# Optimization experiments

Measured on AMD Instinct MI355X. Metric: run time of the kernel, lower is better.

The kernel has to match this reference:

```python
import jax, jax.numpy as jnp
import numpy as np

E, H, B, S = 1024, 16, 8, 512
D = E // H
GRU_BIAS = 2.0  # config['gru_bias']
LN_EPS = 1e-5


def _pos_encoding(seq_len, dim):
    # Transformer-XL style relative positions seq_len-1 .. 0
    pos = jnp.arange(seq_len - 1, -1, -1, dtype=jnp.float32)
    inv_freq = 1.0 / (10000.0 ** (jnp.arange(0, dim, 2, dtype=jnp.float32) / dim))
    ang = pos[:, None] * inv_freq[None, :]              # [S, E/2]
    return jnp.concatenate([jnp.sin(ang), jnp.cos(ang)], axis=-1)  # [S, E]


def _layer_norm(x, g, b):
    m = x.mean(-1, keepdims=True)
    v = ((x - m) ** 2).mean(-1, keepdims=True)
    return (x - m) * jax.lax.rsqrt(v + LN_EPS) * g + b


def _rel_shift(x):
    # x: [B, H, S, S] -> Transformer-XL relative shift
    b, h, s, _ = x.shape
    x = jnp.pad(x, ((0, 0), (0, 0), (0, 0), (1, 0)))
    x = x.reshape(b, h, s + 1, s)[:, :, 1:, :]
    return x


def _gru_gate(x, y, Wr, Ur, Wz, Uz, Wg, Ug):
    # GTrXL gating: r, z gates + candidate h; z biased toward identity by GRU_BIAS
    r = jax.nn.sigmoid(y @ Wr.T + x @ Ur.T)
    z = jax.nn.sigmoid(y @ Wz.T + x @ Uz.T - GRU_BIAS)
    h = jnp.tanh(y @ Wg.T + (r * x) @ Ug.T)
    return (1.0 - z) * x + z * h


def setup_inputs() -> dict:
    rng = jax.random.key(0)
    ks = iter(jax.random.split(rng, 64))
    W = lambda *shape: jax.random.normal(next(ks), shape, jnp.float32) * 0.02
    inp = {
        "query": jax.random.normal(next(ks), (B, S, E), jnp.float32),
        "key": jax.random.normal(next(ks), (B, S, E), jnp.float32),
        "value": jax.random.normal(next(ks), (B, S, E), jnp.float32),
        "mask": jnp.tril(jnp.ones((S, S), dtype=bool)),
        "ln1_g": jnp.ones((E,), jnp.float32), "ln1_b": jnp.zeros((E,), jnp.float32),
        "ln2_g": jnp.ones((E,), jnp.float32), "ln2_b": jnp.zeros((E,), jnp.float32),
        "Wq": W(E, E), "bq": jnp.zeros((E,), jnp.float32),
        "Wk": W(E, E), "bk": jnp.zeros((E,), jnp.float32),
        "Wv": W(E, E), "bv": jnp.zeros((E,), jnp.float32),
        "Wp": W(E, E),
        "Wo": W(E, E), "bo": jnp.zeros((E,), jnp.float32),
        "u_bias": W(H, D), "v_bias": W(H, D),
        "g1_Wr": W(E, E), "g1_Ur": W(E, E), "g1_Wz": W(E, E),
        "g1_Uz": W(E, E), "g1_Wg": W(E, E), "g1_Ug": W(E, E),
        "g2_Wr": W(E, E), "g2_Ur": W(E, E), "g2_Wz": W(E, E),
        "g2_Uz": W(E, E), "g2_Wg": W(E, E), "g2_Ug": W(E, E),
        "fc_W": W(E, E), "fc_b": jnp.zeros((E,), jnp.float32),
    }
    return inp


def reference(query, key, value, mask,
              ln1_g, ln1_b, ln2_g, ln2_b,
              Wq, bq, Wk, bk, Wv, bv, Wp, Wo, bo, u_bias, v_bias,
              g1_Wr, g1_Ur, g1_Wz, g1_Uz, g1_Wg, g1_Ug,
              g2_Wr, g2_Ur, g2_Wz, g2_Uz, g2_Wg, g2_Ug,
              fc_W, fc_b):
    b, s, e = query.shape
    norm_q = _layer_norm(query, ln1_g, ln1_b)
    norm_k = _layer_norm(key, ln1_g, ln1_b)

    q = (norm_q @ Wq.T + bq).reshape(b, s, H, D)
    k = (norm_k @ Wk.T + bk).reshape(b, s, H, D)
    v = (norm_k @ Wv.T + bv).reshape(b, s, H, D)
    r = (_pos_encoding(s, e) @ Wp.T).reshape(s, H, D)      # relative pos keys

    # content term (q + u) k^T and position term (q + v) R^T with rel-shift
    AC = jnp.einsum('bshd,bthd->bhst', q + u_bias, k)
    BD = _rel_shift(jnp.einsum('bshd,thd->bhst', q + v_bias, r))
    score = (AC + BD) / jnp.sqrt(jnp.float32(D))
    score = jnp.where(mask[None, None, :, :], score, jnp.float32(-1e9))
    attn = jax.nn.softmax(score, axis=-1)
    Y = jnp.einsum('bhst,bthd->bshd', attn, v).reshape(b, s, e) @ Wo.T + bo

    out = _gru_gate(query, Y, g1_Wr, g1_Ur, g1_Wz, g1_Uz, g1_Wg, g1_Ug)
    Ef = jax.nn.relu(_layer_norm(out, ln2_g, ln2_b) @ fc_W.T + fc_b)
    out = _gru_gate(out, Ef, g2_Wr, g2_Ur, g2_Wz, g2_Uz, g2_Wg, g2_Ug)
    return out
```

## Files before the change

kernel.cpp:

```cpp
#include <hip/hip_runtime.h>

typedef unsigned short u16;
typedef __attribute__((ext_vector_type(8))) short short8;
typedef __attribute__((ext_vector_type(4))) float f32x4;

#define DEVFN __device__ __forceinline__

constexpr int Bc = 8, Sc = 512, Ec = 1024, Hc = 16, Dc = 64;

DEVFN u16 f2b(float f) {
  union { float f; unsigned u; } a; a.f = f;
  unsigned u = a.u;
  u += 0x7fffu + ((u >> 16) & 1u);
  return (u16)(u >> 16);
}
DEVFN float b2f(u16 h) {
  union { unsigned u; float f; } a; a.u = ((unsigned)h) << 16; return a.f;
}
DEVFN unsigned pack2(float a, float b) {
  return (unsigned)f2b(a) | ((unsigned)f2b(b) << 16);
}
DEVFN float wred_sum(float v) {
  #pragma unroll
  for (int o = 32; o; o >>= 1) v += __shfl_xor(v, o, 64);
  return v;
}
DEVFN void gload16(const void* g, void* l) {
  __builtin_amdgcn_global_load_lds(
      (const __attribute__((address_space(1))) void*)g,
      (__attribute__((address_space(3))) void*)l, 16, 0, 0);
}

struct PtrBundle { const float* src[18]; u16* dst[18]; };

__global__ __launch_bounds__(256) void cvtw_kernel(PtrBundle pb)
{
  int w = blockIdx.y;
  int i = blockIdx.x * 256 + threadIdx.x;
  float4 v = ((const float4*)pb.src[w])[i];
  uint2 o; o.x = pack2(v.x, v.y); o.y = pack2(v.z, v.w);
  ((uint2*)pb.dst[w])[i] = o;
}

struct GemmSeg {
  const u16* A1; const u16* A2;
  const u16* W1; const u16* W2;
  const float* bias;
  const float* bu; const float* bv;
  const u16* xB;
  const float* xF;
  const u16* zB;
  u16* o16a; u16* o16b;
  float* oF;
  int epi;
};
struct GemmDesc { GemmSeg seg[3]; };

template<int TN>
__global__ __launch_bounds__(256) void gemm_f(GemmDesc dd)
{
  constexpr int NI = TN / 32;
  constexpr int BPS = 1024 / TN;
  __shared__ u16 lA[4][128 * 32];
  __shared__ u16 lB[4][TN * 32];
  const int tid = threadIdx.x;

  const GemmSeg s = dd.seg[blockIdx.y / BPS];
  const int n0 = (blockIdx.y % BPS) * TN;
  const int m0 = blockIdx.x * 128;
  const int wid = tid >> 6, lane = tid & 63;
  const int wm = (wid >> 1) * 64, wn = (wid & 1) * (TN / 2);
  const int c15 = lane & 15, g = lane >> 4;
  const int arow = tid >> 2;
  const int ac8 = (((tid & 3) ^ ((tid >> 3) & 3))) * 8;
  const int gs8 = (g ^ ((c15 >> 1) & 3)) * 8;

  f32x4 acc[4][NI];
  #pragma unroll
  for (int mi = 0; mi < 4; ++mi)
    #pragma unroll
    for (int ni = 0; ni < NI; ++ni) acc[mi][ni] = {0.f, 0.f, 0.f, 0.f};

  const int nst = (s.A2 ? 2 : 1) * 32;

  auto stage = [&](int buf, int st) {
    int sg = st >> 5, k0 = (st & 31) << 5;
    const u16* Abase = (sg ? s.A2 : s.A1) + (size_t)m0 * 1024;
    const u16* Wbase = (sg ? s.W2 : s.W1) + (size_t)n0 * 1024;
    gload16(Abase + (size_t)arow * 1024 + k0 + ac8,        &lA[buf][tid * 8]);
    gload16(Abase + (size_t)(arow + 64) * 1024 + k0 + ac8, &lA[buf][2048 + tid * 8]);
    gload16(Wbase + (size_t)arow * 1024 + k0 + ac8,        &lB[buf][tid * 8]);
    if constexpr (TN == 128)
      gload16(Wbase + (size_t)(arow + 64) * 1024 + k0 + ac8, &lB[buf][2048 + tid * 8]);
  };

  stage(0, 0);
  stage(1, 1);
  stage(2, 2);

  for (int st = 0; st < nst; ++st) {
    const int cur = st & 3;
    if (st + 2 < nst) {
      if constexpr (TN == 128) asm volatile("s_waitcnt vmcnt(8)" ::: "memory");
      else                     asm volatile("s_waitcnt vmcnt(6)" ::: "memory");
    } else if (st + 1 < nst) {
      if constexpr (TN == 128) asm volatile("s_waitcnt vmcnt(4)" ::: "memory");
      else                     asm volatile("s_waitcnt vmcnt(3)" ::: "memory");
    } else {
      asm volatile("s_waitcnt vmcnt(0)" ::: "memory");
    }
    __builtin_amdgcn_s_barrier();
    __builtin_amdgcn_sched_barrier(0);

    short8 afr[4], bfr[NI];
    #pragma unroll
    for (int mi = 0; mi < 4; ++mi)
      afr[mi] = *(const short8*)&lA[cur][(wm + mi * 16 + c15) * 32 + gs8];
    #pragma unroll
    for (int ni = 0; ni < NI; ++ni)
      bfr[ni] = *(const short8*)&lB[cur][(wn + ni * 16 + c15) * 32 + gs8];

    if (st + 3 < nst) stage((st + 3) & 3, st + 3);

    #pragma unroll
    for (int mi = 0; mi < 4; ++mi)
      #pragma unroll
      for (int ni = 0; ni < NI; ++ni)
        acc[mi][ni] = __builtin_amdgcn_mfma_f32_16x16x32_bf16(
            afr[mi], bfr[ni], acc[mi][ni], 0, 0, 0);
  }

  const int colb = n0 + wn + c15;
  const int rowb = m0 + wm + (lane >> 4) * 4;
  #pragma unroll
  for (int ni = 0; ni < NI; ++ni) {
    int col = colb + ni * 16;
    float bb = s.bias ? s.bias[col] : 0.f;
    float bu = 0.f, bvv = 0.f;
    if (s.epi == 1) { bu = s.bu[col]; bvv = s.bv[col]; }
    int hI = col >> 6, dI = col & 63;
    int kcd = (dI >> 5) & 1, gd = (dI >> 3) & 3, ed = dI & 7;
    int ntd = dI >> 4, c15d = dI & 15;
    #pragma unroll
    for (int mi = 0; mi < 4; ++mi) {
      int row0 = rowb + mi * 16;
      size_t off0 = (size_t)row0 * 1024 + col;
      float v4[4];
      #pragma unroll
      for (int q = 0; q < 4; ++q) v4[q] = acc[mi][ni][q] + bb;
      switch (s.epi) {
        case 0:
          #pragma unroll
          for (int q = 0; q < 4; ++q) s.o16a[off0 + (size_t)q * 1024] = f2b(v4[q]);
          break;
        case 1:
          #pragma unroll
          for (int q = 0; q < 4; ++q) {
            int ri = row0 + q;
            size_t off = ((size_t)hI << 18) +
                         (((size_t)(((ri >> 4) * 2 + kcd) * 16 + (ri & 15)) * 4 + gd) << 3) + ed;
            s.o16a[off] = f2b((v4[q] + bu)  * 0.125f);
            s.o16b[off] = f2b((v4[q] + bvv) * 0.125f);
          }
          break;
        case 2:
          #pragma unroll
          for (int q = 0; q < 4; ++q) s.o16a[off0 + (size_t)q * 1024] = f2b(v4[q]);
          break;
        case 3:
          #pragma unroll
          for (int q = 0; q < 4; ++q) {
            size_t off = off0 + (size_t)q * 1024;
            float sg1 = 1.f / (1.f + __expf(-v4[q]));
            s.o16a[off] = f2b(sg1 * b2f(s.xB[off]));
          }
          break;
        case 4:
          #pragma unroll
          for (int q = 0; q < 4; ++q) {
            size_t off = off0 + (size_t)q * 1024;
            float z = 1.f / (1.f + __expf(-(b2f(s.zB[off]) - 2.f)));
            float r = (1.f - z) * s.xF[off] + z * tanhf(v4[q]);
            s.oF[off] = r;
            if (s.o16a) s.o16a[off] = f2b(r);
          }
          break;
        case 5:
          #pragma unroll
          for (int q = 0; q < 4; ++q) s.o16a[off0 + (size_t)q * 1024] = f2b(fmaxf(v4[q], 0.f));
          break;
        case 6: {
          int bI = row0 >> 9, j = row0 & 511;
          int kt = j >> 6, jj = j & 63;
          int kcj = jj >> 5, gj = (jj >> 3) & 3, e0 = jj & 7;
          size_t off = ((size_t)((bI * 16 + hI) * 8 + kt) << 12) +
                       (((size_t)((ntd * 2 + kcj) * 16 + c15d) * 4 + gj) << 3) + e0;
          uint2 o; o.x = pack2(v4[0], v4[1]); o.y = pack2(v4[2], v4[3]);
          *(uint2*)(s.o16a + off) = o;
        } break;
        case 7:
          #pragma unroll
          for (int q = 0; q < 4; ++q) {
            int rj = row0 + q;
            int bI = rj >> 9, kt = (rj >> 6) & 7, jr = rj & 63;
            size_t off = ((size_t)((bI * 16 + hI) * 8 + kt) << 12) +
                         (((size_t)(((jr >> 4) * 2 + kcd) * 16 + (jr & 15)) * 4 + gd) << 3) + ed;
            s.o16a[off] = f2b(v4[q]);
          }
          break;
        case 8:
          #pragma unroll
          for (int q = 0; q < 4; ++q) {
            int t = row0 + q;
            size_t off = ((size_t)hI << 14) +
                         (((size_t)(((t >> 4) * 2 + kcd) * 16 + (t & 15)) * 4 + gd) << 3) + ed;
            s.o16a[off] = f2b(v4[q]);
          }
          break;
      }
    }
  }
}

__global__ __launch_bounds__(256) void ln_kernel(
    const float* __restrict__ x, const float* __restrict__ g,
    const float* __restrict__ bb, u16* __restrict__ out,
    u16* __restrict__ out2)
{
  const int row = blockIdx.x, t = threadIdx.x;
  float4 xv = ((const float4*)x)[(size_t)row * 256 + t];
  float s  = xv.x + xv.y + xv.z + xv.w;
  float s2 = xv.x * xv.x + xv.y * xv.y + xv.z * xv.z + xv.w * xv.w;
  s = wred_sum(s); s2 = wred_sum(s2);
  __shared__ float sh[8];
  int wid = t >> 6, lane = t & 63;
  if (lane == 0) { sh[wid] = s; sh[4 + wid] = s2; }
  __syncthreads();
  s  = sh[0] + sh[1] + sh[2] + sh[3];
  s2 = sh[4] + sh[5] + sh[6] + sh[7];
  float mean = s * (1.f / 1024.f);
  float var  = s2 * (1.f / 1024.f) - mean * mean;
  float rstd = rsqrtf(var + 1e-5f);
  float4 gv = ((const float4*)g)[t];
  float4 bv = ((const float4*)bb)[t];
  uint2 o;
  o.x = pack2((xv.x - mean) * rstd * gv.x + bv.x,
              (xv.y - mean) * rstd * gv.y + bv.y);
  o.y = pack2((xv.z - mean) * rstd * gv.z + bv.z,
              (xv.w - mean) * rstd * gv.w + bv.w);
  *(uint2*)&out[(size_t)row * 1024 + t * 4] = o;
  if (out2) {
    uint2 o2; o2.x = pack2(xv.x, xv.y); o2.y = pack2(xv.z, xv.w);
    *(uint2*)&out2[(size_t)row * 1024 + t * 4] = o2;
  }
}

__global__ __launch_bounds__(256) void posenc_kernel(u16* __restrict__ out)
{
  int idx = blockIdx.x * 256 + threadIdx.x;
  int i = idx >> 9, f = idx & 511;
  float pos = (float)(Sc - 1 - i);
  float invf = expf((float)f * -0.017988946039016f);
  float ang = pos * invf;
  out[(size_t)i * 1024 + f]       = f2b(sinf(ang));
  out[(size_t)i * 1024 + 512 + f] = f2b(cosf(ang));
}

__global__ __launch_bounds__(256) void attn_mfma(
    const u16* __restrict__ quF, const u16* __restrict__ qvF,
    const u16* __restrict__ PK, const u16* __restrict__ PVT,
    const u16* __restrict__ RF, u16* __restrict__ out)
{
  __shared__ u16 lK[2][4096];
  __shared__ u16 lVT[2][4096];
  __shared__ u16 PW[4][16 * 72];

  const int tid = threadIdx.x;
  const int wave = tid >> 6, lane = tid & 63;
  const int g = lane >> 4, c15 = lane & 15;
  const int x = blockIdx.x;
  const int h = blockIdx.y, b = blockIdx.z;
  const int qA = x, qB = 7 - x;

  const size_t pkbase = (size_t)(b * 16 + h) << 15;
  const size_t qhead  = (size_t)h << 18;
  const size_t rhead  = (size_t)h << 14;
  const size_t bh_off = ((size_t)b * Sc) * Ec + h * Dc;
  const int fchunk  = (c15 * 4 + g) * 8;
  const int fchunkS = (c15 * 4 + (g ^ ((c15 >> 1) & 3))) * 8;
  const int src8 = (tid ^ ((tid >> 3) & 3)) * 8;

  u16* pw = PW[wave];

  auto stage = [&](int buf, int kt) {
    const u16* ks = PK  + pkbase + ((size_t)kt << 12);
    const u16* vs = PVT + pkbase + ((size_t)kt << 12);
    gload16(ks + src8,        &lK[buf][tid * 8]);
    gload16(ks + 2048 + src8, &lK[buf][2048 + tid * 8]);
    gload16(vs + src8,        &lVT[buf][tid * 8]);
    gload16(vs + 2048 + src8, &lVT[buf][2048 + tid * 8]);
  };

  short8 qa[2], va[2];
  int i0w = qA * 64 + wave * 16;
  {
    int i16g = b * 32 + (i0w >> 4);
    #pragma unroll
    for (int kc = 0; kc < 2; ++kc) {
      size_t off = qhead + ((size_t)(i16g * 2 + kc) * 64) * 8 + fchunk;
      qa[kc] = *(const short8*)(quF + off);
      va[kc] = *(const short8*)(qvF + off);
    }
  }

  f32x4 oacc[4];
  #pragma unroll
  for (int t = 0; t < 4; ++t) oacc[t] = {0.f, 0.f, 0.f, 0.f};
  float m[4], l[4];
  #pragma unroll
  for (int q = 0; q < 4; ++q) { m[q] = -1e30f; l[q] = 0.f; }

  stage(0, 0);
  asm volatile("s_waitcnt vmcnt(0)" ::: "memory");
  __syncthreads();

  for (int s2 = 0; s2 < 9; ++s2) {
    const int buf = s2 & 1;
    const int kt = (s2 <= x) ? s2 : (s2 - x - 1);
    const int j0 = kt * 64;
    if (s2 < 8) {
      int ns = s2 + 1;
      stage(buf ^ 1, (ns <= x) ? ns : (ns - x - 1));
    }

    f32x4 ac[4];
    #pragma unroll
    for (int t = 0; t < 4; ++t) ac[t] = {0.f, 0.f, 0.f, 0.f};
    __builtin_amdgcn_s_setprio(1);
    #pragma unroll
    for (int kc = 0; kc < 2; ++kc)
      #pragma unroll
      for (int nt = 0; nt < 4; ++nt) {
        short8 kb = *(const short8*)&lK[buf][(nt * 2 + kc) * 512 + fchunkS];
        ac[nt] = __builtin_amdgcn_mfma_f32_16x16x32_bf16(qa[kc], kb, ac[nt], 0, 0, 0);
      }

    const int t016 = (496 - i0w + j0) >> 4;
    f32x4 e5[5];
    #pragma unroll
    for (int t = 0; t < 5; ++t) e5[t] = {0.f, 0.f, 0.f, 0.f};
    #pragma unroll
    for (int kc = 0; kc < 2; ++kc)
      #pragma unroll
      for (int nt = 0; nt < 5; ++nt) {
        int t16 = t016 + nt; t16 = t16 > 31 ? 31 : t16;
        short8 rb = *(const short8*)(RF + rhead + (size_t)(t16 * 2 + kc) * 512 + fchunk);
        e5[nt] = __builtin_amdgcn_mfma_f32_16x16x32_bf16(va[kc], rb, e5[nt], 0, 0, 0);
      }
    __builtin_amdgcn_s_setprio(0);

    float rot[5][4];
    #pragma unroll
    for (int q = 0; q < 4; ++q) {
      int src = (lane & 48) | ((15 - (g * 4 + q) + c15) & 15);
      #pragma unroll
      for (int nt = 0; nt < 5; ++nt)
        rot[nt][q] = __shfl(e5[nt][q], src, 64);
    }

    float s[4][4];
    #pragma unroll
    for (int ct = 0; ct < 4; ++ct) {
      int jcol = j0 + ct * 16 + c15;
      #pragma unroll
      for (int q = 0; q < 4; ++q) {
        int r = g * 4 + q;
        int u = 15 - r + c15;
        float bd = (u >> 4) ? rot[ct + 1][q] : rot[ct][q];
        float sv = ac[ct][q] + bd;
        s[ct][q] = (jcol <= i0w + r) ? sv : -1e30f;
      }
    }

    float mnew[4], csc[4];
    #pragma unroll
    for (int q = 0; q < 4; ++q) {
      float mx = fmaxf(fmaxf(s[0][q], s[1][q]), fmaxf(s[2][q], s[3][q]));
      #pragma unroll
      for (int o = 8; o; o >>= 1) mx = fmaxf(mx, __shfl_xor(mx, o, 64));
      mnew[q] = fmaxf(m[q], mx);
      csc[q] = __expf(m[q] - mnew[q]);
      m[q] = mnew[q];
    }
    float rs[4] = {0.f, 0.f, 0.f, 0.f};
    float p[4][4];
    #pragma unroll
    for (int ct = 0; ct < 4; ++ct)
      #pragma unroll
      for (int q = 0; q < 4; ++q) {
        p[ct][q] = __expf(s[ct][q] - mnew[q]);
        rs[q] += p[ct][q];
      }
    #pragma unroll
    for (int q = 0; q < 4; ++q) {
      float t = rs[q];
      #pragma unroll
      for (int o = 8; o; o >>= 1) t += __shfl_xor(t, o, 64);
      l[q] = l[q] * csc[q] + t;
      #pragma unroll
      for (int ct = 0; ct < 4; ++ct) oacc[ct][q] *= csc[q];
    }

    #pragma unroll
    for (int ct = 0; ct < 4; ++ct)
      #pragma unroll
      for (int q = 0; q < 4; ++q)
        pw[(g * 4 + q) * 72 + ct * 16 + c15] = f2b(p[ct][q]);

    __builtin_amdgcn_s_setprio(1);
    #pragma unroll
    for (int kc = 0; kc < 2; ++kc) {
      short8 pa = *(const short8*)&pw[c15 * 72 + kc * 32 + g * 8];
      #pragma unroll
      for (int nt = 0; nt < 4; ++nt) {
        short8 vb8 = *(const short8*)&lVT[buf][(nt * 2 + kc) * 512 + fchunkS];
        oacc[nt] = __builtin_amdgcn_mfma_f32_16x16x32_bf16(pa, vb8, oacc[nt], 0, 0, 0);
      }
    }
    __builtin_amdgcn_s_setprio(0);

    if (s2 == x) {
      #pragma unroll
      for (int q = 0; q < 4; ++q) {
        float rl = 1.f / l[q];
        size_t ro = bh_off + (size_t)(i0w + g * 4 + q) * Ec;
        #pragma unroll
        for (int ct = 0; ct < 4; ++ct)
          out[ro + ct * 16 + c15] = f2b(oacc[ct][q] * rl);
      }
      i0w = qB * 64 + wave * 16;
      int i16g = b * 32 + (i0w >> 4);
      #pragma unroll
      for (int kc = 0; kc < 2; ++kc) {
        size_t off = qhead + ((size_t)(i16g * 2 + kc) * 64) * 8 + fchunk;
        qa[kc] = *(const short8*)(quF + off);
        va[kc] = *(const short8*)(qvF + off);
      }
      #pragma unroll
      for (int t = 0; t < 4; ++t) oacc[t] = {0.f, 0.f, 0.f, 0.f};
      #pragma unroll
      for (int q = 0; q < 4; ++q) { m[q] = -1e30f; l[q] = 0.f; }
    }

    asm volatile("s_waitcnt vmcnt(0)" ::: "memory");
    __syncthreads();
  }

  #pragma unroll
  for (int q = 0; q < 4; ++q) {
    float rl = 1.f / l[q];
    size_t ro = bh_off + (size_t)(i0w + g * 4 + q) * Ec;
    #pragma unroll
    for (int ct = 0; ct < 4; ++ct)
      out[ro + ct * 16 + c15] = f2b(oacc[ct][q] * rl);
  }
}

extern "C" void kernel_launch(void* const* d_in, const int* in_sizes, int n_in,
                              void* d_out, int out_size, void* d_ws, size_t ws_size,
                              hipStream_t stream) {
  (void)in_sizes; (void)n_in; (void)out_size; (void)ws_size;

  const float* query = (const float*)d_in[0];
  const float* key   = (const float*)d_in[1];
  const float* ln1_g = (const float*)d_in[4];
  const float* ln1_b = (const float*)d_in[5];
  const float* ln2_g = (const float*)d_in[6];
  const float* ln2_b = (const float*)d_in[7];
  const float* Wq = (const float*)d_in[8];   const float* bq = (const float*)d_in[9];
  const float* Wk = (const float*)d_in[10];  const float* bk = (const float*)d_in[11];
  const float* Wv = (const float*)d_in[12];  const float* bv_in = (const float*)d_in[13];
  const float* Wp = (const float*)d_in[14];
  const float* Wo = (const float*)d_in[15];  const float* bo = (const float*)d_in[16];
  const float* u_bias = (const float*)d_in[17];
  const float* v_bias = (const float*)d_in[18];
  const float* fc_W = (const float*)d_in[31]; const float* fc_b = (const float*)d_in[32];

  const size_t MB = 1ull << 20;
  char* ws = (char*)d_ws;
  u16* wb[18];
  for (int i = 0; i < 18; ++i) wb[i] = (u16*)(ws + (size_t)i * 2 * MB);
  u16*   normq16 = (u16*)(ws + 36 * MB);
  u16*   normk16 = (u16*)(ws + 44 * MB);
  u16*   xq16    = (u16*)(ws + 52 * MB);
  u16*   pos16   = (u16*)(ws + 60 * MB);
  u16*   rF16    = (u16*)(ws + 61 * MB);
  u16*   quF16   = (u16*)(ws + 62 * MB);
  u16*   qvF16   = (u16*)(ws + 70 * MB);
  u16*   pk16    = (u16*)(ws + 78 * MB);
  u16*   pvt16   = (u16*)(ws + 86 * MB);
  float* out1    = (float*)(ws + 94 * MB);
  u16*   att16   = normq16;
  u16*   Y16     = normk16;
  u16*   rx16    = normq16;
  u16*   out116  = quF16;
  u16*   Ef16    = qvF16;
  u16*   ln2o16  = xq16;
  u16*   tB16    = pk16;

  PtrBundle pb;
  const float* wsrc[18] = {Wq, Wk, Wv, Wp, Wo, fc_W,
                           (const float*)d_in[19], (const float*)d_in[20],
                           (const float*)d_in[21], (const float*)d_in[22],
                           (const float*)d_in[23], (const float*)d_in[24],
                           (const float*)d_in[25], (const float*)d_in[26],
                           (const float*)d_in[27], (const float*)d_in[28],
                           (const float*)d_in[29], (const float*)d_in[30]};
  for (int i = 0; i < 18; ++i) { pb.src[i] = wsrc[i]; pb.dst[i] = wb[i]; }
  cvtw_kernel<<<dim3(1024, 18), 256, 0, stream>>>(pb);

  ln_kernel<<<4096, 256, 0, stream>>>(query, ln1_g, ln1_b, normq16, xq16);
  ln_kernel<<<4096, 256, 0, stream>>>(key,   ln1_g, ln1_b, normk16, nullptr);
  posenc_kernel<<<1024, 256, 0, stream>>>(pos16);

  GemmSeg z{}; GemmDesc d;

  d.seg[0] = z; d.seg[0].A1 = normq16; d.seg[0].W1 = wb[0]; d.seg[0].bias = bq;
  d.seg[0].bu = u_bias; d.seg[0].bv = v_bias;
  d.seg[0].o16a = quF16; d.seg[0].o16b = qvF16; d.seg[0].epi = 1;
  d.seg[1] = z; d.seg[1].A1 = normk16; d.seg[1].W1 = wb[1]; d.seg[1].bias = bk;
  d.seg[1].o16a = pk16; d.seg[1].epi = 7;
  d.seg[2] = z; d.seg[2].A1 = normk16; d.seg[2].W1 = wb[2]; d.seg[2].bias = bv_in;
  d.seg[2].o16a = pvt16; d.seg[2].epi = 6;
  gemm_f<128><<<dim3(32, 24), 256, 0, stream>>>(d);

  d.seg[0] = z; d.seg[0].A1 = pos16; d.seg[0].W1 = wb[3];
  d.seg[0].o16a = rF16; d.seg[0].epi = 8;
  gemm_f<64><<<dim3(4, 16), 256, 0, stream>>>(d);

  attn_mfma<<<dim3(4, 16, 8), 256, 0, stream>>>(quF16, qvF16, pk16, pvt16,
                                                rF16, att16);

  d.seg[0] = z; d.seg[0].A1 = att16; d.seg[0].W1 = wb[4]; d.seg[0].bias = bo;
  d.seg[0].o16a = Y16; d.seg[0].epi = 0;
  gemm_f<64><<<dim3(32, 16), 256, 0, stream>>>(d);

  d.seg[0] = z; d.seg[0].A1 = Y16; d.seg[0].A2 = xq16;
  d.seg[0].W1 = wb[6]; d.seg[0].W2 = wb[7];
  d.seg[0].xB = xq16; d.seg[0].o16a = rx16; d.seg[0].epi = 3;
  d.seg[1] = z; d.seg[1].A1 = Y16; d.seg[1].A2 = xq16;
  d.seg[1].W1 = wb[8]; d.seg[1].W2 = wb[9];
  d.seg[1].o16a = tB16; d.seg[1].epi = 2;
  gemm_f<128><<<dim3(32, 16), 256, 0, stream>>>(d);

  d.seg[0] = z; d.seg[0].A1 = Y16; d.seg[0].A2 = rx16;
  d.seg[0].W1 = wb[10]; d.seg[0].W2 = wb[11];
  d.seg[0].xF = query; d.seg[0].zB = tB16;
  d.seg[0].oF = out1; d.seg[0].o16a = out116; d.seg[0].epi = 4;
  gemm_f<64><<<dim3(32, 16), 256, 0, stream>>>(d);

  ln_kernel<<<4096, 256, 0, stream>>>(out1, ln2_g, ln2_b, ln2o16, nullptr);
  d.seg[0] = z; d.seg[0].A1 = ln2o16; d.seg[0].W1 = wb[5]; d.seg[0].bias = fc_b;
  d.seg[0].o16a = Ef16; d.seg[0].epi = 5;
  gemm_f<64><<<dim3(32, 16), 256, 0, stream>>>(d);

  d.seg[0] = z; d.seg[0].A1 = Ef16; d.seg[0].A2 = out116;
  d.seg[0].W1 = wb[12]; d.seg[0].W2 = wb[13];
  d.seg[0].xB = out116; d.seg[0].o16a = rx16; d.seg[0].epi = 3;
  d.seg[1] = z; d.seg[1].A1 = Ef16; d.seg[1].A2 = out116;
  d.seg[1].W1 = wb[14]; d.seg[1].W2 = wb[15];
  d.seg[1].o16a = tB16; d.seg[1].epi = 2;
  gemm_f<128><<<dim3(32, 16), 256, 0, stream>>>(d);

  d.seg[0] = z; d.seg[0].A1 = Ef16; d.seg[0].A2 = rx16;
  d.seg[0].W1 = wb[16]; d.seg[0].W2 = wb[17];
  d.seg[0].xF = out1; d.seg[0].zB = tB16;
  d.seg[0].oF = (float*)d_out; d.seg[0].epi = 4;
  gemm_f<64><<<dim3(32, 16), 256, 0, stream>>>(d);
}
```

Before: 369.4 us.

## Use 8-wave blocks with triple buffering for 128-wide GEMM tiles

The 128x128-tile GEMM variant now launches 512 threads (8 waves), each wave computing a 64x32 sub-tile instead of 64x64. This halves the accumulator registers per wave and the global loads per thread per stage. The LDS ring for that variant shrinks from 4 to 3 buffers with a prefetch distance of 2, which lowers LDS use so more blocks can be resident. The trade-off is a shallower prefetch pipeline and more barrier participants per block.

```diff
diff --git a/kernel.cpp b/kernel.cpp
--- a/kernel.cpp
+++ b/kernel.cpp
@@ -57,29 +57,31 @@
 struct GemmDesc { GemmSeg seg[3]; };
 
 template<int TN>
-__global__ __launch_bounds__(256) void gemm_f(GemmDesc dd)
+__global__ __launch_bounds__(TN == 128 ? 512 : 256) void gemm_f(GemmDesc dd)
 {
-  constexpr int NI = TN / 32;
+  constexpr int NBUF = (TN == 128) ? 3 : 4;
   constexpr int BPS = 1024 / TN;
-  __shared__ u16 lA[4][128 * 32];
-  __shared__ u16 lB[4][TN * 32];
+  __shared__ u16 lA[NBUF][128 * 32];
+  __shared__ u16 lB[NBUF][TN * 32];
   const int tid = threadIdx.x;
 
   const GemmSeg s = dd.seg[blockIdx.y / BPS];
   const int n0 = (blockIdx.y % BPS) * TN;
   const int m0 = blockIdx.x * 128;
   const int wid = tid >> 6, lane = tid & 63;
-  const int wm = (wid >> 1) * 64, wn = (wid & 1) * (TN / 2);
+  int wm, wn;
+  if constexpr (TN == 128) { wm = (wid >> 2) * 64; wn = (wid & 3) * 32; }
+  else                     { wm = (wid >> 1) * 64; wn = (wid & 1) * 32; }
   const int c15 = lane & 15, g = lane >> 4;
   const int arow = tid >> 2;
   const int ac8 = (((tid & 3) ^ ((tid >> 3) & 3))) * 8;
   const int gs8 = (g ^ ((c15 >> 1) & 3)) * 8;
 
-  f32x4 acc[4][NI];
+  f32x4 acc[4][2];
   #pragma unroll
   for (int mi = 0; mi < 4; ++mi)
     #pragma unroll
-    for (int ni = 0; ni < NI; ++ni) acc[mi][ni] = {0.f, 0.f, 0.f, 0.f};
+    for (int ni = 0; ni < 2; ++ni) acc[mi][ni] = {0.f, 0.f, 0.f, 0.f};
 
   const int nst = (s.A2 ? 2 : 1) * 32;
 
@@ -87,53 +89,78 @@
     int sg = st >> 5, k0 = (st & 31) << 5;
     const u16* Abase = (sg ? s.A2 : s.A1) + (size_t)m0 * 1024;
     const u16* Wbase = (sg ? s.W2 : s.W1) + (size_t)n0 * 1024;
-    gload16(Abase + (size_t)arow * 1024 + k0 + ac8,        &lA[buf][tid * 8]);
-    gload16(Abase + (size_t)(arow + 64) * 1024 + k0 + ac8, &lA[buf][2048 + tid * 8]);
-    gload16(Wbase + (size_t)arow * 1024 + k0 + ac8,        &lB[buf][tid * 8]);
-    if constexpr (TN == 128)
-      gload16(Wbase + (size_t)(arow + 64) * 1024 + k0 + ac8, &lB[buf][2048 + tid * 8]);
+    if constexpr (TN == 128) {
+      gload16(Abase + (size_t)arow * 1024 + k0 + ac8, &lA[buf][tid * 8]);
+      gload16(Wbase + (size_t)arow * 1024 + k0 + ac8, &lB[buf][tid * 8]);
+    } else {
+      gload16(Abase + (size_t)arow * 1024 + k0 + ac8,        &lA[buf][tid * 8]);
+      gload16(Abase + (size_t)(arow + 64) * 1024 + k0 + ac8, &lA[buf][2048 + tid * 8]);
+      gload16(Wbase + (size_t)arow * 1024 + k0 + ac8,        &lB[buf][tid * 8]);
+    }
   };
 
-  stage(0, 0);
-  stage(1, 1);
-  stage(2, 2);
-
-  for (int st = 0; st < nst; ++st) {
-    const int cur = st & 3;
-    if (st + 2 < nst) {
-      if constexpr (TN == 128) asm volatile("s_waitcnt vmcnt(8)" ::: "memory");
-      else                     asm volatile("s_waitcnt vmcnt(6)" ::: "memory");
-    } else if (st + 1 < nst) {
-      if constexpr (TN == 128) asm volatile("s_waitcnt vmcnt(4)" ::: "memory");
-      else                     asm volatile("s_waitcnt vmcnt(3)" ::: "memory");
-    } else {
-      asm volatile("s_waitcnt vmcnt(0)" ::: "memory");
-    }
-    __builtin_amdgcn_s_barrier();
-    __builtin_amdgcn_sched_barrier(0);
-
-    short8 afr[4], bfr[NI];
-    #pragma unroll
-    for (int mi = 0; mi < 4; ++mi)
-      afr[mi] = *(const short8*)&lA[cur][(wm + mi * 16 + c15) * 32 + gs8];
-    #pragma unroll
-    for (int ni = 0; ni < NI; ++ni)
-      bfr[ni] = *(const short8*)&lB[cur][(wn + ni * 16 + c15) * 32 + gs8];
-
-    if (st + 3 < nst) stage((st + 3) & 3, st + 3);
-
-    #pragma unroll
-    for (int mi = 0; mi < 4; ++mi)
-      #pragma unroll
-      for (int ni = 0; ni < NI; ++ni)
-        acc[mi][ni] = __builtin_amdgcn_mfma_f32_16x16x32_bf16(
-            afr[mi], bfr[ni], acc[mi][ni], 0, 0, 0);
+  if constexpr (TN == 128) {
+    stage(0, 0);
+    stage(1, 1);
+    for (int st = 0; st < nst; ++st) {
+      const int cur = st % 3;
+      if (st + 1 < nst) asm volatile("s_waitcnt vmcnt(2)" ::: "memory");
+      else              asm volatile("s_waitcnt vmcnt(0)" ::: "memory");
+      __builtin_amdgcn_s_barrier();
+      __builtin_amdgcn_sched_barrier(0);
+
+      short8 afr[4], bfr[2];
+      #pragma unroll
+      for (int mi = 0; mi < 4; ++mi)
+        afr[mi] = *(const short8*)&lA[cur][(wm + mi * 16 + c15) * 32 + gs8];
+      #pragma unroll
+      for (int ni = 0; ni < 2; ++ni)
+        bfr[ni] = *(const short8*)&lB[cur][(wn + ni * 16 + c15) * 32 + gs8];
+
+      if (st + 2 < nst) stage((st + 2) % 3, st + 2);
+
+      #pragma unroll
+      for (int mi = 0; mi < 4; ++mi)
+        #pragma unroll
+        for (int ni = 0; ni < 2; ++ni)
+          acc[mi][ni] = __builtin_amdgcn_mfma_f32_16x16x32_bf16(
+              afr[mi], bfr[ni], acc[mi][ni], 0, 0, 0);
+    }
+  } else {
+    stage(0, 0);
+    stage(1, 1);
+    stage(2, 2);
+    for (int st = 0; st < nst; ++st) {
+      const int cur = st & 3;
+      if (st + 2 < nst)      asm volatile("s_waitcnt vmcnt(6)" ::: "memory");
+      else if (st + 1 < nst) asm volatile("s_waitcnt vmcnt(3)" ::: "memory");
+      else                   asm volatile("s_waitcnt vmcnt(0)" ::: "memory");
+      __builtin_amdgcn_s_barrier();
+      __builtin_amdgcn_sched_barrier(0);
+
+      short8 afr[4], bfr[2];
+      #pragma unroll
+      for (int mi = 0; mi < 4; ++mi)
+        afr[mi] = *(const short8*)&lA[cur][(wm + mi * 16 + c15) * 32 + gs8];
+      #pragma unroll
+      for (int ni = 0; ni < 2; ++ni)
+        bfr[ni] = *(const short8*)&lB[cur][(wn + ni * 16 + c15) * 32 + gs8];
+
+      if (st + 3 < nst) stage((st + 3) & 3, st + 3);
+
+      #pragma unroll
+      for (int mi = 0; mi < 4; ++mi)
+        #pragma unroll
+        for (int ni = 0; ni < 2; ++ni)
+          acc[mi][ni] = __builtin_amdgcn_mfma_f32_16x16x32_bf16(
+              afr[mi], bfr[ni], acc[mi][ni], 0, 0, 0);
+    }
   }
 
   const int colb = n0 + wn + c15;
   const int rowb = m0 + wm + (lane >> 4) * 4;
   #pragma unroll
-  for (int ni = 0; ni < NI; ++ni) {
+  for (int ni = 0; ni < 2; ++ni) {
     int col = colb + ni * 16;
     float bb = s.bias ? s.bias[col] : 0.f;
     float bu = 0.f, bvv = 0.f;
@@ -532,7 +559,7 @@
   d.seg[1].o16a = pk16; d.seg[1].epi = 7;
   d.seg[2] = z; d.seg[2].A1 = normk16; d.seg[2].W1 = wb[2]; d.seg[2].bias = bv_in;
   d.seg[2].o16a = pvt16; d.seg[2].epi = 6;
-  gemm_f<128><<<dim3(32, 24), 256, 0, stream>>>(d);
+  gemm_f<128><<<dim3(32, 24), 512, 0, stream>>>(d);
 
   d.seg[0] = z; d.seg[0].A1 = pos16; d.seg[0].W1 = wb[3];
   d.seg[0].o16a = rF16; d.seg[0].epi = 8;
@@ -551,7 +578,7 @@
   d.seg[1] = z; d.seg[1].A1 = Y16; d.seg[1].A2 = xq16;
   d.seg[1].W1 = wb[8]; d.seg[1].W2 = wb[9];
   d.seg[1].o16a = tB16; d.seg[1].epi = 2;
-  gemm_f<128><<<dim3(32, 16), 256, 0, stream>>>(d);
+  gemm_f<128><<<dim3(32, 16), 512, 0, stream>>>(d);
 
   d.seg[0] = z; d.seg[0].A1 = Y16; d.seg[0].A2 = rx16;
   d.seg[0].W1 = wb[10]; d.seg[0].W2 = wb[11];
@@ -570,7 +597,7 @@
   d.seg[1] = z; d.seg[1].A1 = Ef16; d.seg[1].A2 = out116;
   d.seg[1].W1 = wb[14]; d.seg[1].W2 = wb[15];
   d.seg[1].o16a = tB16; d.seg[1].epi = 2;
-  gemm_f<128><<<dim3(32, 16), 256, 0, stream>>>(d);
+  gemm_f<128><<<dim3(32, 16), 512, 0, stream>>>(d);
 
   d.seg[0] = z; d.seg[0].A1 = Ef16; d.seg[0].A2 = rx16;
   d.seg[0].W1 = wb[16]; d.seg[0].W2 = wb[17];
```

After: 333.7 us. 9.7% less time.
